# Kernel optimization log

Measured on AMD Instinct MI355X. Metric: run time of the kernel, lower is better.

## Reference

```python
import jax, jax.numpy as jnp
import numpy as np

N_NODES = 50000
N_EDGES = 800000
IN_DIM = 64
HID = 256
EDGE_DIM = 6
NEG_SLOPE = 0.2


def setup_inputs() -> dict:
    key = jax.random.key(0)
    ks = jax.random.split(key, 16)
    glorot = lambda k, shp: jax.random.normal(k, shp, jnp.float32) * jnp.sqrt(2.0 / (shp[0] + shp[-1]))
    x = jax.random.normal(ks[0], (N_NODES, IN_DIM), jnp.float32)
    edge_index = jax.random.randint(ks[1], (2, N_EDGES), 0, N_NODES, dtype=jnp.int32)
    edge_attr = jax.random.normal(ks[2], (N_EDGES, EDGE_DIM), jnp.float32)
    return {
        "x": x,
        "edge_index": edge_index,
        "edge_attr": edge_attr,
        # layer 1 (heads=1)
        "W1": glorot(ks[3], (IN_DIM, HID)),
        "att_src1": glorot(ks[4], (HID,)),
        "att_dst1": glorot(ks[5], (HID,)),
        "We1": glorot(ks[6], (EDGE_DIM, HID)),
        "att_e1": glorot(ks[7], (HID,)),
        "b1": jnp.zeros((HID,), jnp.float32),
        # layer 2
        "W2": glorot(ks[8], (HID, HID)),
        "att_src2": glorot(ks[9], (HID,)),
        "att_dst2": glorot(ks[10], (HID,)),
        "We2": glorot(ks[11], (EDGE_DIM, HID)),
        "att_e2": glorot(ks[12], (HID,)),
        "b2": jnp.zeros((HID,), jnp.float32),
    }


def gat_conv(x, src, dst, edge_attr, W, att_src, att_dst, We, att_e, b):
    # PyG GATConv, heads=1, add_self_loops=False, edge features in attention only
    h = x @ W                              # [N, C]
    a_src = h @ att_src                    # [N]
    a_dst = h @ att_dst                    # [N]
    a_edge = (edge_attr @ We) @ att_e      # [E]
    alpha = a_src[src] + a_dst[dst] + a_edge            # [E]
    alpha = jax.nn.leaky_relu(alpha, NEG_SLOPE)
    # softmax over edges sharing the same destination node
    amax = jax.ops.segment_max(alpha, dst, num_segments=N_NODES)
    amax = jnp.where(jnp.isneginf(amax), 0.0, amax)
    ex = jnp.exp(alpha - amax[dst])
    denom = jax.ops.segment_sum(ex, dst, num_segments=N_NODES)
    alpha = ex / (denom[dst] + 1e-16)
    msg = h[src] * alpha[:, None]          # [E, C]
    out = jax.ops.segment_sum(msg, dst, num_segments=N_NODES)  # [N, C]
    return out + b


def reference(x, edge_index, edge_attr, W1, att_src1, att_dst1, We1, att_e1, b1,
              W2, att_src2, att_dst2, We2, att_e2, b2):
    src, dst = edge_index[0], edge_index[1]
    h = jax.nn.relu(gat_conv(x, src, dst, edge_attr, W1, att_src1, att_dst1, We1, att_e1, b1))
    # dropout(p=0.2) is identity in eval mode
    out = gat_conv(h, src, dst, edge_attr, W2, att_src2, att_dst2, We2, att_e2, b2)
    return out  # out_proj is Identity (out_dim=None)
```

## Files before the change

kernel.cpp:

```cpp
#include <hip/hip_runtime.h>
#include <hip/hip_bf16.h>

#define N_NODES_C 50000
#define N_EDGES_C 800000
#define IN_DIM_C 64
#define HID_C 256
#define EDGE_DIM_C 6
#define NEG_SLOPE_C 0.2f

typedef short short8 __attribute__((ext_vector_type(8)));
typedef float f32x4 __attribute__((ext_vector_type(4)));

static __device__ __forceinline__ float b2f(unsigned short u) {
    union { unsigned int i; float f; } x;
    x.i = ((unsigned int)u) << 16;
    return x.f;
}
static __device__ __forceinline__ unsigned short f2b(float f) {
    union { __hip_bfloat16 h; unsigned short u; } x;
    x.h = __float2bfloat16(f);
    return x.u;
}

__global__ void k_prep(const float* __restrict__ W1, const float* __restrict__ W2,
                       unsigned short* __restrict__ W1t, unsigned short* __restrict__ W2t) {
    int i = blockIdx.x * blockDim.x + threadIdx.x;
    if (i < IN_DIM_C * HID_C) {
        int k = i >> 8, n = i & 255;
        W1t[n * IN_DIM_C + k] = f2b(W1[i]);
    }
    if (i < HID_C * HID_C) {
        int k = i >> 8, n = i & 255;
        W2t[n * HID_C + k] = f2b(W2[i]);
    }
}

__global__ void k_v12(const float* __restrict__ We1, const float* __restrict__ atte1,
                      const float* __restrict__ We2, const float* __restrict__ atte2,
                      float* __restrict__ v) {
    __shared__ float red[256];
    int tid = threadIdx.x;
    for (int layer = 0; layer < 2; ++layer) {
        const float* We = layer ? We2 : We1;
        const float* ae = layer ? atte2 : atte1;
        for (int k = 0; k < EDGE_DIM_C; ++k) {
            red[tid] = We[k * HID_C + tid] * ae[tid];
            __syncthreads();
            for (int s = 128; s > 0; s >>= 1) {
                if (tid < s) red[tid] += red[tid + s];
                __syncthreads();
            }
            if (tid == 0) v[layer * 8 + k] = red[0];
            __syncthreads();
        }
    }
}

__global__ void k_hist(const int* __restrict__ dst, int* __restrict__ deg) {
    int e = blockIdx.x * blockDim.x + threadIdx.x;
    if (e < N_EDGES_C) atomicAdd(&deg[dst[e]], 1);
}

__global__ void k_scan1(const int* __restrict__ deg, int* __restrict__ offs,
                        int* __restrict__ bsum) {
    __shared__ int tmp[256];
    int b = blockIdx.x, tid = threadIdx.x;
    int i = b * 256 + tid;
    int v = (i < N_NODES_C) ? deg[i] : 0;
    tmp[tid] = v;
    __syncthreads();
    for (int d = 1; d < 256; d <<= 1) {
        int t = (tid >= d) ? tmp[tid - d] : 0;
        __syncthreads();
        tmp[tid] += t;
        __syncthreads();
    }
    if (i < N_NODES_C) offs[i] = tmp[tid] - v;
    if (tid == 255) bsum[b] = tmp[255];
}
__global__ void k_scan2(const int* __restrict__ bsum, int* __restrict__ boff, int nb) {
    __shared__ int tmp[256];
    int tid = threadIdx.x;
    int v = (tid < nb) ? bsum[tid] : 0;
    tmp[tid] = v;
    __syncthreads();
    for (int d = 1; d < 256; d <<= 1) {
        int t = (tid >= d) ? tmp[tid - d] : 0;
        __syncthreads();
        tmp[tid] += t;
        __syncthreads();
    }
    if (tid < nb) boff[tid] = tmp[tid] - v;
}
__global__ void k_scan3(int* __restrict__ offs, const int* __restrict__ boff) {
    int b = blockIdx.x, tid = threadIdx.x;
    int i = b * 256 + tid;
    if (i < N_NODES_C) offs[i] += boff[b];
    if (i == 0) offs[N_NODES_C] = N_EDGES_C;
}

__global__ void k_scatter(const int* __restrict__ src, const int* __restrict__ dst,
                          const float* __restrict__ eattr, const int* __restrict__ offs,
                          int* __restrict__ cur, const float* __restrict__ v,
                          int* __restrict__ ssrc, int* __restrict__ sdst,
                          float* __restrict__ sae1, float* __restrict__ sae2) {
    int e = blockIdx.x * blockDim.x + threadIdx.x;
    if (e >= N_EDGES_C) return;
    int d = dst[e];
    int pos = offs[d] + atomicAdd(&cur[d], 1);
    ssrc[pos] = src[e];
    sdst[pos] = d;
    float a1 = 0.f, a2 = 0.f;
#pragma unroll
    for (int k = 0; k < EDGE_DIM_C; ++k) {
        float ea = eattr[e * EDGE_DIM_C + k];
        a1 += ea * v[k];
        a2 += ea * v[8 + k];
    }
    sae1[pos] = a1;
    sae2[pos] = a2;
}

template <int KT, bool SRCF32>
__global__ __launch_bounds__(256) void k_gemm_mfma(const void* __restrict__ Xv,
                                                   const unsigned short* __restrict__ Wt,
                                                   unsigned short* __restrict__ H) {
    __shared__ unsigned short As[64 * 64];
    __shared__ unsigned short Bs[256 * 64];
    int tid = threadIdx.x;
    int w = tid >> 6, l = tid & 63;
    int lr = l & 15, lg = l >> 4;
    long mbase = (long)blockIdx.x * 64;

    f32x4 acc[4][4];
#pragma unroll
    for (int mi = 0; mi < 4; ++mi)
#pragma unroll
        for (int ni = 0; ni < 4; ++ni) acc[mi][ni] = (f32x4){0.f, 0.f, 0.f, 0.f};

    for (int k0 = 0; k0 < KT; k0 += 64) {
#pragma unroll
        for (int p = 0; p < 2; ++p) {
            int r = p * 32 + (tid >> 3);
            int c8 = tid & 7;
            long row = mbase + r;
            short8 val = {0, 0, 0, 0, 0, 0, 0, 0};
            if (row < N_NODES_C) {
                if (SRCF32) {
                    const float* Xf = (const float*)Xv;
                    const f32x4* p4 = (const f32x4*)&Xf[row * KT + k0 + c8 * 8];
                    f32x4 a0 = p4[0], a1 = p4[1];
#pragma unroll
                    for (int q = 0; q < 4; ++q) val[q] = (short)f2b(a0[q]);
#pragma unroll
                    for (int q = 0; q < 4; ++q) val[4 + q] = (short)f2b(a1[q]);
                } else {
                    const unsigned short* Xb = (const unsigned short*)Xv;
                    val = *(const short8*)&Xb[row * KT + k0 + c8 * 8];
                }
            }
            *(short8*)&As[r * 64 + ((c8 ^ (r & 7)) * 8)] = val;
        }
        {
            int n = tid;
#pragma unroll
            for (int c8 = 0; c8 < 8; ++c8) {
                *(short8*)&Bs[n * 64 + ((c8 ^ (n & 7)) * 8)] =
                    *(const short8*)&Wt[(long)n * KT + k0 + c8 * 8];
            }
        }
        __syncthreads();
#pragma unroll
        for (int kk = 0; kk < 2; ++kk) {
            int cblk = kk * 4 + lg;
            short8 a[4], b[4];
#pragma unroll
            for (int mi = 0; mi < 4; ++mi) {
                int R = mi * 16 + lr;
                a[mi] = *(const short8*)&As[R * 64 + ((cblk ^ (R & 7)) * 8)];
            }
#pragma unroll
            for (int ni = 0; ni < 4; ++ni) {
                int Nr = w * 64 + ni * 16 + lr;
                b[ni] = *(const short8*)&Bs[Nr * 64 + ((cblk ^ (Nr & 7)) * 8)];
            }
#pragma unroll
            for (int mi = 0; mi < 4; ++mi)
#pragma unroll
                for (int ni = 0; ni < 4; ++ni)
                    acc[mi][ni] = __builtin_amdgcn_mfma_f32_16x16x32_bf16(a[mi], b[ni],
                                                                          acc[mi][ni], 0, 0, 0);
        }
        __syncthreads();
    }
#pragma unroll
    for (int mi = 0; mi < 4; ++mi) {
#pragma unroll
        for (int r = 0; r < 4; ++r) {
            long row = mbase + mi * 16 + lg * 4 + r;
            if (row < N_NODES_C) {
#pragma unroll
                for (int ni = 0; ni < 4; ++ni) {
                    H[row * HID_C + w * 64 + ni * 16 + lr] = f2b(acc[mi][ni][r]);
                }
            }
        }
    }
}

__global__ void k_dots(const unsigned short* __restrict__ H, const float* __restrict__ att_s,
                       const float* __restrict__ att_d, float* __restrict__ asrc,
                       float* __restrict__ adst) {
    int tid = threadIdx.x;
    int w = tid >> 6, l = tid & 63, sub = l >> 5;
    int node = blockIdx.x * 8 + w * 2 + sub;
    if (node >= N_NODES_C) return;
    int c8 = (l & 31) * 8;
    short8 hv = *(const short8*)&H[(long)node * HID_C + c8];
    const f32x4* as4 = (const f32x4*)&att_s[c8];
    const f32x4* ad4 = (const f32x4*)&att_d[c8];
    f32x4 s0 = as4[0], s1 = as4[1], d0 = ad4[0], d1 = ad4[1];
    float s = 0.f, d = 0.f;
#pragma unroll
    for (int q = 0; q < 4; ++q) {
        float h = b2f((unsigned short)hv[q]);
        s += h * s0[q];
        d += h * d0[q];
    }
#pragma unroll
    for (int q = 0; q < 4; ++q) {
        float h = b2f((unsigned short)hv[4 + q]);
        s += h * s1[q];
        d += h * d1[q];
    }
    for (int off = 16; off > 0; off >>= 1) {
        s += __shfl_down(s, off, 32);
        d += __shfl_down(d, off, 32);
    }
    if ((l & 31) == 0) {
        asrc[node] = s;
        adst[node] = d;
    }
}

__global__ void k_wts(const int* __restrict__ ssrc, const int* __restrict__ sdst,
                      const float* __restrict__ sae, const float* __restrict__ asrc,
                      const float* __restrict__ adst, float* __restrict__ wts) {
    int p = blockIdx.x * blockDim.x + threadIdx.x;
    if (p >= N_EDGES_C) return;
    float a = asrc[ssrc[p]] + adst[sdst[p]] + sae[p];
    a = (a > 0.f) ? a : NEG_SLOPE_C * a;
    wts[p] = __expf(a);
}

__global__ __launch_bounds__(256) void k_aggr2(const int* __restrict__ offs,
                                               const int* __restrict__ ssrc,
                                               const float* __restrict__ wts,
                                               const unsigned short* __restrict__ H,
                                               const float* __restrict__ bias,
                                               void* __restrict__ outp, int mode) {
    int tid = threadIdx.x;
    int hw = tid >> 5;
    int l = tid & 31;
    int node = blockIdx.x * 8 + hw;
    if (node >= N_NODES_C) return;
    int off0 = offs[node];
    int deg = offs[node + 1] - off0;

    float s = 0.f;
    for (int j = l; j < deg; j += 32) s += wts[off0 + j];
#pragma unroll
    for (int o = 16; o > 0; o >>= 1) s += __shfl_xor(s, o, 32);
    float inv = 1.0f / (s + 1e-16f);

    int c8 = l * 8;
    float acc[8];
#pragma unroll
    for (int q = 0; q < 8; ++q) acc[q] = 0.f;

    int j = 0;
    for (; j + 1 < deg; j += 2) {
        int s0 = ssrc[off0 + j];
        int s1 = ssrc[off0 + j + 1];
        float w0 = wts[off0 + j];
        float w1 = wts[off0 + j + 1];
        short8 h0 = *(const short8*)&H[(long)s0 * HID_C + c8];
        short8 h1 = *(const short8*)&H[(long)s1 * HID_C + c8];
#pragma unroll
        for (int q = 0; q < 8; ++q)
            acc[q] += w0 * b2f((unsigned short)h0[q]) + w1 * b2f((unsigned short)h1[q]);
    }
    if (j < deg) {
        int s0 = ssrc[off0 + j];
        float w0 = wts[off0 + j];
        short8 h0 = *(const short8*)&H[(long)s0 * HID_C + c8];
#pragma unroll
        for (int q = 0; q < 8; ++q) acc[q] += w0 * b2f((unsigned short)h0[q]);
    }

    const f32x4* b4 = (const f32x4*)&bias[c8];
    f32x4 bv0 = b4[0], bv1 = b4[1];
    if (mode == 1) {
        unsigned short* o16 = (unsigned short*)outp;
        short8 r;
#pragma unroll
        for (int q = 0; q < 4; ++q)
            r[q] = (short)f2b(fmaxf(acc[q] * inv + bv0[q], 0.f));
#pragma unroll
        for (int q = 0; q < 4; ++q)
            r[4 + q] = (short)f2b(fmaxf(acc[4 + q] * inv + bv1[q], 0.f));
        *(short8*)&o16[(long)node * HID_C + c8] = r;
    } else {
        float* o32 = (float*)outp;
        f32x4 r0, r1;
#pragma unroll
        for (int q = 0; q < 4; ++q) r0[q] = acc[q] * inv + bv0[q];
#pragma unroll
        for (int q = 0; q < 4; ++q) r1[q] = acc[4 + q] * inv + bv1[q];
        *(f32x4*)&o32[(long)node * HID_C + c8] = r0;
        *(f32x4*)&o32[(long)node * HID_C + c8 + 4] = r1;
    }
}

extern "C" void kernel_launch(void* const* d_in, const int* in_sizes, int n_in,
                              void* d_out, int out_size, void* d_ws, size_t ws_size,
                              hipStream_t stream) {
    const float* x     = (const float*)d_in[0];
    const int*   ei    = (const int*)d_in[1];
    const float* eattr = (const float*)d_in[2];
    const float* W1    = (const float*)d_in[3];
    const float* atts1 = (const float*)d_in[4];
    const float* attd1 = (const float*)d_in[5];
    const float* We1   = (const float*)d_in[6];
    const float* atte1 = (const float*)d_in[7];
    const float* b1    = (const float*)d_in[8];
    const float* W2    = (const float*)d_in[9];
    const float* atts2 = (const float*)d_in[10];
    const float* attd2 = (const float*)d_in[11];
    const float* We2   = (const float*)d_in[12];
    const float* atte2 = (const float*)d_in[13];
    const float* b2    = (const float*)d_in[14];
    float* out = (float*)d_out;

    char* ws = (char*)d_ws;
    size_t off = 0;
    auto alloc = [&](size_t bytes) -> void* {
        void* p = ws + off;
        off = (off + bytes + 255) & ~(size_t)255;
        return p;
    };
    int*   deg  = (int*)alloc((size_t)N_NODES_C * 4);
    int*   offs = (int*)alloc(((size_t)N_NODES_C + 1) * 4);
    int*   cur  = (int*)alloc((size_t)N_NODES_C * 4);
    int*   ssrc = (int*)alloc((size_t)N_EDGES_C * 4);
    int*   sdst = (int*)alloc((size_t)N_EDGES_C * 4);
    float* sae1 = (float*)alloc((size_t)N_EDGES_C * 4);
    float* sae2 = (float*)alloc((size_t)N_EDGES_C * 4);
    float* wts  = (float*)alloc((size_t)N_EDGES_C * 4);
    float* asrc = (float*)alloc((size_t)N_NODES_C * 4);
    float* adst = (float*)alloc((size_t)N_NODES_C * 4);
    float* v    = (float*)alloc(64);
    int*   bsum = (int*)alloc(256 * 4);
    int*   boff = (int*)alloc(257 * 4);
    unsigned short* W1t = (unsigned short*)alloc((size_t)HID_C * IN_DIM_C * 2);
    unsigned short* W2t = (unsigned short*)alloc((size_t)HID_C * HID_C * 2);
    unsigned short* h1  = (unsigned short*)alloc((size_t)N_NODES_C * HID_C * 2);
    unsigned short* g1  = (unsigned short*)alloc((size_t)N_NODES_C * HID_C * 2);

    const int* src = ei;
    const int* dst = ei + N_EDGES_C;
    int nb = (N_NODES_C + 255) / 256;

    hipMemsetAsync(deg, 0, (size_t)N_NODES_C * 4, stream);
    hipMemsetAsync(cur, 0, (size_t)N_NODES_C * 4, stream);

    k_prep<<<HID_C * HID_C / 256, 256, 0, stream>>>(W1, W2, W1t, W2t);
    k_v12<<<1, 256, 0, stream>>>(We1, atte1, We2, atte2, v);
    k_hist<<<(N_EDGES_C + 255) / 256, 256, 0, stream>>>(dst, deg);
    k_scan1<<<nb, 256, 0, stream>>>(deg, offs, bsum);
    k_scan2<<<1, 256, 0, stream>>>(bsum, boff, nb);
    k_scan3<<<nb, 256, 0, stream>>>(offs, boff);
    k_scatter<<<(N_EDGES_C + 255) / 256, 256, 0, stream>>>(src, dst, eattr, offs, cur, v,
                                                           ssrc, sdst, sae1, sae2);

    int gemm_grid = (N_NODES_C + 63) / 64;
    k_gemm_mfma<IN_DIM_C, true><<<gemm_grid, 256, 0, stream>>>(x, W1t, h1);
    k_dots<<<N_NODES_C / 8, 256, 0, stream>>>(h1, atts1, attd1, asrc, adst);
    k_wts<<<(N_EDGES_C + 255) / 256, 256, 0, stream>>>(ssrc, sdst, sae1, asrc, adst, wts);
    k_aggr2<<<N_NODES_C / 8, 256, 0, stream>>>(offs, ssrc, wts, h1, b1, g1, 1);
    k_gemm_mfma<HID_C, false><<<gemm_grid, 256, 0, stream>>>(g1, W2t, h1);
    k_dots<<<N_NODES_C / 8, 256, 0, stream>>>(h1, atts2, attd2, asrc, adst);
    k_wts<<<(N_EDGES_C + 255) / 256, 256, 0, stream>>>(ssrc, sdst, sae2, asrc, adst, wts);
    k_aggr2<<<N_NODES_C / 8, 256, 0, stream>>>(offs, ssrc, wts, h1, b2, out, 0);
}
```

Measured before the change: 307.3 us.

## Fuse edge-weight computation into aggregation and split CSR scatter into perm+gather

Removes the separate k_wts kernels by computing leaky-relu/exp edge weights inside k_aggr2. The first 64 weights per node are cached in registers and broadcast with shuffles, and higher-degree edges are recomputed. The CSR build is split into an atomic permutation pass (cursor initialised by copying offsets) followed by a coalesced gather pass, which drops the sdst array. The aggregation loop is unrolled to 4 neighbours for more memory parallelism. The cost is extra shuffles and some recomputation of weights.

```diff
diff --git a/kernel.cpp b/kernel.cpp
--- a/kernel.cpp
+++ b/kernel.cpp
@@ -99,17 +99,22 @@
     if (i == 0) offs[N_NODES_C] = N_EDGES_C;
 }
 
-__global__ void k_scatter(const int* __restrict__ src, const int* __restrict__ dst,
-                          const float* __restrict__ eattr, const int* __restrict__ offs,
-                          int* __restrict__ cur, const float* __restrict__ v,
-                          int* __restrict__ ssrc, int* __restrict__ sdst,
-                          float* __restrict__ sae1, float* __restrict__ sae2) {
+__global__ void k_perm(const int* __restrict__ dst, int* __restrict__ cur,
+                       int* __restrict__ perm) {
     int e = blockIdx.x * blockDim.x + threadIdx.x;
     if (e >= N_EDGES_C) return;
-    int d = dst[e];
-    int pos = offs[d] + atomicAdd(&cur[d], 1);
-    ssrc[pos] = src[e];
-    sdst[pos] = d;
+    int pos = atomicAdd(&cur[dst[e]], 1);
+    perm[pos] = e;
+}
+
+__global__ void k_gather(const int* __restrict__ perm, const int* __restrict__ src,
+                         const float* __restrict__ eattr, const float* __restrict__ v,
+                         int* __restrict__ ssrc, float* __restrict__ sae1,
+                         float* __restrict__ sae2) {
+    int p = blockIdx.x * blockDim.x + threadIdx.x;
+    if (p >= N_EDGES_C) return;
+    int e = perm[p];
+    ssrc[p] = src[e];
     float a1 = 0.f, a2 = 0.f;
 #pragma unroll
     for (int k = 0; k < EDGE_DIM_C; ++k) {
@@ -117,8 +122,8 @@
         a1 += ea * v[k];
         a2 += ea * v[8 + k];
     }
-    sae1[pos] = a1;
-    sae2[pos] = a2;
+    sae1[p] = a1;
+    sae2[p] = a2;
 }
 
 template <int KT, bool SRCF32>
@@ -243,19 +248,11 @@
     }
 }
 
-__global__ void k_wts(const int* __restrict__ ssrc, const int* __restrict__ sdst,
-                      const float* __restrict__ sae, const float* __restrict__ asrc,
-                      const float* __restrict__ adst, float* __restrict__ wts) {
-    int p = blockIdx.x * blockDim.x + threadIdx.x;
-    if (p >= N_EDGES_C) return;
-    float a = asrc[ssrc[p]] + adst[sdst[p]] + sae[p];
-    a = (a > 0.f) ? a : NEG_SLOPE_C * a;
-    wts[p] = __expf(a);
-}
-
 __global__ __launch_bounds__(256) void k_aggr2(const int* __restrict__ offs,
                                                const int* __restrict__ ssrc,
-                                               const float* __restrict__ wts,
+                                               const float* __restrict__ sae,
+                                               const float* __restrict__ asrc,
+                                               const float* __restrict__ adst,
                                                const unsigned short* __restrict__ H,
                                                const float* __restrict__ bias,
                                                void* __restrict__ outp, int mode) {
@@ -266,9 +263,29 @@
     if (node >= N_NODES_C) return;
     int off0 = offs[node];
     int deg = offs[node + 1] - off0;
-
-    float s = 0.f;
-    for (int j = l; j < deg; j += 32) s += wts[off0 + j];
+    float adi = adst[node];
+
+    int sidx0 = 0, sidx1 = 0;
+    float w0 = 0.f, w1 = 0.f;
+    if (l < deg) {
+        sidx0 = ssrc[off0 + l];
+        float a = asrc[sidx0] + adi + sae[off0 + l];
+        a = (a > 0.f) ? a : NEG_SLOPE_C * a;
+        w0 = __expf(a);
+    }
+    if (32 + l < deg) {
+        sidx1 = ssrc[off0 + 32 + l];
+        float a = asrc[sidx1] + adi + sae[off0 + 32 + l];
+        a = (a > 0.f) ? a : NEG_SLOPE_C * a;
+        w1 = __expf(a);
+    }
+    float s = w0 + w1;
+    for (int j = 64 + l; j < deg; j += 32) {
+        int si = ssrc[off0 + j];
+        float a = asrc[si] + adi + sae[off0 + j];
+        a = (a > 0.f) ? a : NEG_SLOPE_C * a;
+        s += __expf(a);
+    }
 #pragma unroll
     for (int o = 16; o > 0; o >>= 1) s += __shfl_xor(s, o, 32);
     float inv = 1.0f / (s + 1e-16f);
@@ -278,24 +295,45 @@
 #pragma unroll
     for (int q = 0; q < 8; ++q) acc[q] = 0.f;
 
+    auto fetch = [&](int j, int& si, float& wv) {
+        if (j < 32) {
+            si = __shfl(sidx0, j, 32);
+            wv = __shfl(w0, j, 32);
+        } else if (j < 64) {
+            si = __shfl(sidx1, j - 32, 32);
+            wv = __shfl(w1, j - 32, 32);
+        } else {
+            si = ssrc[off0 + j];
+            float a = asrc[si] + adi + sae[off0 + j];
+            a = (a > 0.f) ? a : NEG_SLOPE_C * a;
+            wv = __expf(a);
+        }
+    };
+
     int j = 0;
-    for (; j + 1 < deg; j += 2) {
-        int s0 = ssrc[off0 + j];
-        int s1 = ssrc[off0 + j + 1];
-        float w0 = wts[off0 + j];
-        float w1 = wts[off0 + j + 1];
-        short8 h0 = *(const short8*)&H[(long)s0 * HID_C + c8];
-        short8 h1 = *(const short8*)&H[(long)s1 * HID_C + c8];
+    for (; j + 3 < deg; j += 4) {
+        int i0, i1, i2, i3;
+        float u0, u1, u2, u3;
+        fetch(j, i0, u0);
+        fetch(j + 1, i1, u1);
+        fetch(j + 2, i2, u2);
+        fetch(j + 3, i3, u3);
+        short8 h0 = *(const short8*)&H[(long)i0 * HID_C + c8];
+        short8 h1 = *(const short8*)&H[(long)i1 * HID_C + c8];
+        short8 h2 = *(const short8*)&H[(long)i2 * HID_C + c8];
+        short8 h3 = *(const short8*)&H[(long)i3 * HID_C + c8];
 #pragma unroll
         for (int q = 0; q < 8; ++q)
-            acc[q] += w0 * b2f((unsigned short)h0[q]) + w1 * b2f((unsigned short)h1[q]);
-    }
-    if (j < deg) {
-        int s0 = ssrc[off0 + j];
-        float w0 = wts[off0 + j];
-        short8 h0 = *(const short8*)&H[(long)s0 * HID_C + c8];
-#pragma unroll
-        for (int q = 0; q < 8; ++q) acc[q] += w0 * b2f((unsigned short)h0[q]);
+            acc[q] += u0 * b2f((unsigned short)h0[q]) + u1 * b2f((unsigned short)h1[q]) +
+                      u2 * b2f((unsigned short)h2[q]) + u3 * b2f((unsigned short)h3[q]);
+    }
+    for (; j < deg; ++j) {
+        int i0;
+        float u0;
+        fetch(j, i0, u0);
+        short8 h0 = *(const short8*)&H[(long)i0 * HID_C + c8];
+#pragma unroll
+        for (int q = 0; q < 8; ++q) acc[q] += u0 * b2f((unsigned short)h0[q]);
     }
 
     const f32x4* b4 = (const f32x4*)&bias[c8];
@@ -352,11 +390,10 @@
     int*   deg  = (int*)alloc((size_t)N_NODES_C * 4);
     int*   offs = (int*)alloc(((size_t)N_NODES_C + 1) * 4);
     int*   cur  = (int*)alloc((size_t)N_NODES_C * 4);
+    int*   perm = (int*)alloc((size_t)N_EDGES_C * 4);
     int*   ssrc = (int*)alloc((size_t)N_EDGES_C * 4);
-    int*   sdst = (int*)alloc((size_t)N_EDGES_C * 4);
     float* sae1 = (float*)alloc((size_t)N_EDGES_C * 4);
     float* sae2 = (float*)alloc((size_t)N_EDGES_C * 4);
-    float* wts  = (float*)alloc((size_t)N_EDGES_C * 4);
     float* asrc = (float*)alloc((size_t)N_NODES_C * 4);
     float* adst = (float*)alloc((size_t)N_NODES_C * 4);
     float* v    = (float*)alloc(64);
@@ -372,7 +409,6 @@
     int nb = (N_NODES_C + 255) / 256;
 
     hipMemsetAsync(deg, 0, (size_t)N_NODES_C * 4, stream);
-    hipMemsetAsync(cur, 0, (size_t)N_NODES_C * 4, stream);
 
     k_prep<<<HID_C * HID_C / 256, 256, 0, stream>>>(W1, W2, W1t, W2t);
     k_v12<<<1, 256, 0, stream>>>(We1, atte1, We2, atte2, v);
@@ -380,16 +416,15 @@
     k_scan1<<<nb, 256, 0, stream>>>(deg, offs, bsum);
     k_scan2<<<1, 256, 0, stream>>>(bsum, boff, nb);
     k_scan3<<<nb, 256, 0, stream>>>(offs, boff);
-    k_scatter<<<(N_EDGES_C + 255) / 256, 256, 0, stream>>>(src, dst, eattr, offs, cur, v,
-                                                           ssrc, sdst, sae1, sae2);
+    hipMemcpyAsync(cur, offs, (size_t)N_NODES_C * 4, hipMemcpyDeviceToDevice, stream);
+    k_perm<<<(N_EDGES_C + 255) / 256, 256, 0, stream>>>(dst, cur, perm);
+    k_gather<<<(N_EDGES_C + 255) / 256, 256, 0, stream>>>(perm, src, eattr, v, ssrc, sae1, sae2);
 
     int gemm_grid = (N_NODES_C + 63) / 64;
     k_gemm_mfma<IN_DIM_C, true><<<gemm_grid, 256, 0, stream>>>(x, W1t, h1);
     k_dots<<<N_NODES_C / 8, 256, 0, stream>>>(h1, atts1, attd1, asrc, adst);
-    k_wts<<<(N_EDGES_C + 255) / 256, 256, 0, stream>>>(ssrc, sdst, sae1, asrc, adst, wts);
-    k_aggr2<<<N_NODES_C / 8, 256, 0, stream>>>(offs, ssrc, wts, h1, b1, g1, 1);
+    k_aggr2<<<N_NODES_C / 8, 256, 0, stream>>>(offs, ssrc, sae1, asrc, adst, h1, b1, g1, 1);
     k_gemm_mfma<HID_C, false><<<gemm_grid, 256, 0, stream>>>(g1, W2t, h1);
     k_dots<<<N_NODES_C / 8, 256, 0, stream>>>(h1, atts2, attd2, asrc, adst);
-    k_wts<<<(N_EDGES_C + 255) / 256, 256, 0, stream>>>(ssrc, sdst, sae2, asrc, adst, wts);
-    k_aggr2<<<N_NODES_C / 8, 256, 0, stream>>>(offs, ssrc, wts, h1, b2, out, 0);
-}
+    k_aggr2<<<N_NODES_C / 8, 256, 0, stream>>>(offs, ssrc, sae2, asrc, adst, h1, b2, out, 0);
+}
```

Result: no change. 304.7 us (-0.8%).
